# Kernel optimization log

Measured on AMD Instinct MI355X. Metric: run time of the kernel, lower is better.

The kernel has to match this reference:

```python
import jax, jax.numpy as jnp
import numpy as np

WS = 7      # window size
SS = 3      # shift size = WS // 2
NH = 12     # num heads
EPS = 1e-5  # LayerNorm eps


def _ln(x, g, b):
    m = jnp.mean(x, axis=-1, keepdims=True)
    v = jnp.var(x, axis=-1, keepdims=True)
    return (x - m) * jax.lax.rsqrt(v + EPS) * g + b


def _rel_index(ws):
    # relative position index (N, N), N = ws*ws (static, numpy)
    coords = np.stack(np.meshgrid(np.arange(ws), np.arange(ws), indexing='ij')).reshape(2, -1)
    rel = (coords[:, :, None] - coords[:, None, :]).transpose(1, 2, 0).copy()
    rel[:, :, 0] += ws - 1
    rel[:, :, 1] += ws - 1
    rel[:, :, 0] *= 2 * ws - 1
    return rel.sum(-1)


def _attn_mask(H, W, ws, ss):
    # SW-MSA mask (nW, N, N): -100 where tokens come from different shifted regions
    img = np.zeros((H, W), np.float32)
    cnt = 0
    sls = (slice(0, -ws), slice(-ws, -ss), slice(-ss, None))
    for hs in sls:
        for wsl in sls:
            img[hs, wsl] = cnt
            cnt += 1
    win = img.reshape(H // ws, ws, W // ws, ws).transpose(0, 2, 1, 3).reshape(-1, ws * ws)
    d = win[:, None, :] - win[:, :, None]
    return np.where(d != 0, -100.0, 0.0).astype(np.float32)


def _forward(x, rel_bias_table, qkv_w, qkv_b, proj_w, proj_b,
             norm1_w, norm1_b, norm2_w, norm2_b,
             mlp_w1, mlp_b1, mlp_w2, mlp_b2, h, w):
    B, L, C = x.shape
    ws, ss, nH = WS, SS, NH
    hd = C // nH
    N = ws * ws
    scale = hd ** -0.5
    nWh, nWw = h // ws, w // ws
    nW = nWh * nWw

    shortcut = x
    y = _ln(x, norm1_w, norm1_b).reshape(B, h, w, C)
    # cyclic shift (SW-MSA)
    y = jnp.roll(y, (-ss, -ss), axis=(1, 2))
    # window partition -> (B*nW, N, C)
    y = y.reshape(B, nWh, ws, nWw, ws, C).transpose(0, 1, 3, 2, 4, 5).reshape(-1, N, C)

    qkv = (y @ qkv_w + qkv_b).reshape(-1, N, 3, nH, hd).transpose(2, 0, 3, 1, 4)
    q, k, v = qkv[0] * scale, qkv[1], qkv[2]  # (Bw, nH, N, hd)

    attn = jnp.einsum('bhnd,bhmd->bhnm', q, k)  # (Bw, nH, N, N)
    # learned relative position bias
    idx = jnp.asarray(_rel_index(ws))  # (N, N)
    bias = rel_bias_table[idx].transpose(2, 0, 1)[None]  # (1, nH, N, N)
    attn = attn + bias
    # shifted-window mask
    mask = jnp.asarray(_attn_mask(h, w, ws, ss))  # (nW, N, N)
    attn = attn.reshape(B, nW, nH, N, N) + mask[None, :, None]
    attn = jax.nn.softmax(attn.reshape(-1, nH, N, N), axis=-1)

    out = jnp.einsum('bhnm,bhmd->bhnd', attn, v).transpose(0, 2, 1, 3).reshape(-1, N, C)
    out = out @ proj_w + proj_b
    # window reverse + un-shift
    out = out.reshape(B, nWh, nWw, ws, ws, C).transpose(0, 1, 3, 2, 4, 5).reshape(B, h, w, C)
    out = jnp.roll(out, (ss, ss), axis=(1, 2)).reshape(B, L, C)

    x = shortcut + out
    y2 = _ln(x, norm2_w, norm2_b)
    mlp = jax.nn.gelu(y2 @ mlp_w1 + mlp_b1, approximate=False) @ mlp_w2 + mlp_b2
    return x + mlp


def setup_inputs() -> dict:
    key = jax.random.key(0)
    ks = jax.random.split(key, 8)
    B, H, W, C = 32, 56, 56, 384
    hid = int(C * 4.0)
    ws, nH = WS, NH
    inp = {
        'x': jax.random.normal(ks[0], (B, H * W, C), jnp.float32),
        'rel_bias_table': 0.02 * jax.random.normal(ks[1], ((2 * ws - 1) * (2 * ws - 1), nH), jnp.float32),
        'qkv_w': 0.02 * jax.random.normal(ks[2], (C, 3 * C), jnp.float32),
        'qkv_b': jnp.zeros((3 * C,), jnp.float32),
        'proj_w': 0.02 * jax.random.normal(ks[3], (C, C), jnp.float32),
        'proj_b': jnp.zeros((C,), jnp.float32),
        'norm1_w': jnp.ones((C,), jnp.float32),
        'norm1_b': jnp.zeros((C,), jnp.float32),
        'norm2_w': jnp.ones((C,), jnp.float32),
        'norm2_b': jnp.zeros((C,), jnp.float32),
        'mlp_w1': 0.02 * jax.random.normal(ks[4], (C, hid), jnp.float32),
        'mlp_b1': jnp.zeros((hid,), jnp.float32),
        'mlp_w2': 0.02 * jax.random.normal(ks[5], (hid, C), jnp.float32),
        'mlp_b2': jnp.zeros((C,), jnp.float32),
        'h': H,
        'w': W,
    }
    return inp


def reference(x, rel_bias_table, qkv_w, qkv_b, proj_w, proj_b,
              norm1_w, norm1_b, norm2_w, norm2_b,
              mlp_w1, mlp_b1, mlp_w2, mlp_b2, h, w):
    return _forward(x, rel_bias_table, qkv_w, qkv_b, proj_w, proj_b,
                    norm1_w, norm1_b, norm2_w, norm2_b,
                    mlp_w1, mlp_b1, mlp_w2, mlp_b2, h, w)
```

## Files before the change

### kernel.cpp

```cpp
#include <hip/hip_runtime.h>

typedef unsigned short u16;
typedef unsigned int u32;
typedef short s8v __attribute__((ext_vector_type(8)));
typedef float f4 __attribute__((ext_vector_type(4)));

#define GL16(g, l) __builtin_amdgcn_global_load_lds((const __attribute__((address_space(1))) u32*)(g), (__attribute__((address_space(3))) u32*)(l), 16, 0, 0)

__device__ __forceinline__ u16 f2bf(float f){
  u32 u = __builtin_bit_cast(u32, f);
  u32 r = u + 0x7fffu + ((u >> 16) & 1u);
  return (u16)(r >> 16);
}

__device__ __forceinline__ u32 pk_bf16(float lo, float hi){
  u32 r;
  asm("v_cvt_pk_bf16_f32 %0, %1, %2" : "=v"(r) : "v"(lo), "v"(hi));
  return r;
}

__device__ __forceinline__ float gelu_f(float x){
  float y = fabsf(x) * 0.70710678118654752f;
  float t = __builtin_amdgcn_rcpf(1.f + 0.3275911f*y);
  float p = ((((1.061405429f*t - 1.453152027f)*t + 1.421413741f)*t - 0.284496736f)*t + 0.254829592f)*t;
  float er = 1.f - p*__expf(-y*y);
  er = copysignf(er, x);
  return 0.5f*x*(1.f + er);
}

__device__ __forceinline__ int win_to_src(int orow){
  int wi = orow / 49;
  int n  = orow - wi*49;
  int b  = wi >> 6;
  int wq = wi & 63;
  int wh = wq >> 3, ww = wq & 7;
  int r = n / 7, c = n - r*7;
  int hh = wh*7 + r + 3; if (hh >= 56) hh -= 56;
  int wp = ww*7 + c + 3; if (wp >= 56) wp -= 56;
  return (b*56 + hh)*56 + wp;
}

__global__ void sentinel_kernel(float* o){ o[0] = 1.0e9f; }

__global__ void transpose_cast(const float* __restrict__ in, u16* __restrict__ out,
                               int K, int N, float scale, int scale_lim){
  __shared__ float tile[16][17];
  int kb = blockIdx.x*16, nb = blockIdx.y*16;
  int tx = threadIdx.x, ty = threadIdx.y;
  int k = kb + ty, n = nb + tx;
  tile[ty][tx] = (k < K && n < N) ? in[(size_t)k*N + n] : 0.f;
  __syncthreads();
  int on = nb + ty, ok = kb + tx;
  if (on < N && ok < K){
    float v = tile[tx][ty];
    if (on < scale_lim) v *= scale;
    out[(size_t)on*K + ok] = f2bf(v);
  }
}

__global__ void scale_bias(const float* __restrict__ in, float* __restrict__ out,
                           int n, float s, int lim){
  int i = blockIdx.x*256 + threadIdx.x;
  if (i < n) out[i] = in[i] * (i < lim ? s : 1.f);
}

__global__ void build_biasmask(const float* __restrict__ table, float* __restrict__ bm){
  int wq = blockIdx.x, h = blockIdx.y;
  int wh = wq >> 3, ww = wq & 7;
  float* o = bm + (size_t)(wq*12 + h) * 4096;
  for (int i = threadIdx.x; i < 4096; i += 256){
    int m = i >> 6, n = i & 63;
    float v;
    if (m < 49 && n < 49){
      int rm = m/7, cm = m - rm*7;
      int rn = n/7, cn = n - rn*7;
      int idx = (rm - rn + 6)*13 + (cm - cn + 6);
      v = table[idx*12 + h];
      int ym = wh*7 + rm, xm = ww*7 + cm;
      int yn = wh*7 + rn, xn = ww*7 + cn;
      int lm = (ym < 49 ? 0 : (ym < 53 ? 1 : 2))*3 + (xm < 49 ? 0 : (xm < 53 ? 1 : 2));
      int ln = (yn < 49 ? 0 : (yn < 53 ? 1 : 2))*3 + (xn < 49 ? 0 : (xn < 53 ? 1 : 2));
      if (lm != ln) v += -100.f;
    } else {
      v = -1e9f;
    }
    o[i] = v;
  }
}

template<bool GATHER>
__global__ __launch_bounds__(256) void ln_kernel(const float* __restrict__ x,
    const float* __restrict__ g, const float* __restrict__ b,
    u16* __restrict__ y, int nrows)
{
  int row = blockIdx.x*4 + (threadIdx.x >> 6);
  int lane = threadIdx.x & 63;
  if (row >= nrows) return;
  int src = GATHER ? win_to_src(row) : row;
  const float* xr = x + (size_t)src*384;
  float v[6];
  float s = 0.f, s2 = 0.f;
  #pragma unroll
  for (int p = 0; p < 3; p++){
    float2 t = *(const float2*)(xr + p*128 + lane*2);
    v[p*2] = t.x; v[p*2+1] = t.y;
    s += t.x + t.y; s2 += t.x*t.x + t.y*t.y;
  }
  #pragma unroll
  for (int off = 32; off; off >>= 1){
    s  += __shfl_xor(s,  off);
    s2 += __shfl_xor(s2, off);
  }
  float mean = s * (1.f/384.f);
  float var  = s2 * (1.f/384.f) - mean*mean;
  float rs   = rsqrtf(var + 1e-5f);
  u16* yr = y + (size_t)row*384;
  #pragma unroll
  for (int p = 0; p < 3; p++){
    int c = p*128 + lane*2;
    float a0 = (v[p*2]   - mean)*rs*g[c]   + b[c];
    float a1 = (v[p*2+1] - mean)*rs*g[c+1] + b[c+1];
    *(u32*)(yr + c) = pk_bf16(a0, a1);
  }
}

template<int MODE, int NF>
__global__ __launch_bounds__(256) void gemm_bf16(
    const u16* __restrict__ A, const u16* __restrict__ Bt,
    const float* __restrict__ bias, const float* __restrict__ resid,
    void* __restrict__ outp, int K, int N, int gn)
{
  constexpr int TN = NF * 32;
  __shared__ u16 As[2][128*64];
  __shared__ u16 Bs[2][TN*64];
  const int tid  = threadIdx.x;
  const int lane = tid & 63, wv = tid >> 6;
  const int wr = wv >> 1, wc = wv & 1;
  const int l15 = lane & 15, lhi = lane >> 4;
  const int sw  = l15 & 7;

  int total = gridDim.x;
  int flat  = blockIdx.x;
  int swz   = flat;
  if ((total & 7) == 0){
    int cpx = total >> 3;
    swz = (flat & 7)*cpx + (flat >> 3);
  }
  int bm = swz / gn, bn = swz - bm*gn;
  const size_t m0 = (size_t)bm * 128;
  const int n0 = bn * TN;

  f4 acc[4][NF] = {};

  auto stage = [&](int buf, int kt){
    #pragma unroll
    for (int it = 0; it < 4; it++){
      int c = it*256 + tid;
      int row = c >> 3;
      int col = (((c & 7) ^ (row & 7))) * 8;
      const u16* ga = A + (m0 + (size_t)row)*K + kt*64 + col;
      GL16(ga, &As[buf][(it*256 + wv*64)*8]);
    }
    #pragma unroll
    for (int it = 0; it < NF; it++){
      int c = it*256 + tid;
      int row = c >> 3;
      int col = (((c & 7) ^ (row & 7))) * 8;
      const u16* gb = Bt + ((size_t)n0 + row)*K + kt*64 + col;
      GL16(gb, &Bs[buf][(it*256 + wv*64)*8]);
    }
  };

  const int nk = K >> 6;
  stage(0, 0);
  for (int kt = 0; kt < nk; kt++){
    const int cur = kt & 1;
    if (kt + 1 < nk){
      stage(cur ^ 1, kt + 1);
      asm volatile("s_waitcnt vmcnt(8)" ::: "memory");
    } else {
      asm volatile("s_waitcnt vmcnt(0)" ::: "memory");
    }
    __builtin_amdgcn_s_barrier();
    #pragma unroll
    for (int kk = 0; kk < 2; kk++){
      s8v a[4], bb[NF];
      #pragma unroll
      for (int mi = 0; mi < 4; mi++)
        a[mi] = *(const s8v*)&As[cur][(wr*64 + mi*16 + l15)*64 + ((kk*4 + lhi) ^ sw)*8];
      #pragma unroll
      for (int ni = 0; ni < NF; ni++)
        bb[ni] = *(const s8v*)&Bs[cur][(wc*NF*16 + ni*16 + l15)*64 + ((kk*4 + lhi) ^ sw)*8];
      #pragma unroll
      for (int mi = 0; mi < 4; mi++)
        #pragma unroll
        for (int ni = 0; ni < NF; ni++)
          acc[mi][ni] = __builtin_amdgcn_mfma_f32_16x16x32_bf16(bb[ni], a[mi], acc[mi][ni], 0, 0, 0);
    }
    asm volatile("s_waitcnt lgkmcnt(0)" ::: "memory");
    __builtin_amdgcn_s_barrier();
  }

  #pragma unroll
  for (int mi = 0; mi < 4; mi++){
    int m = (int)m0 + wr*64 + mi*16 + l15;
    int src = 0;
    if constexpr (MODE == 1) src = win_to_src(m);
    #pragma unroll
    for (int ni = 0; ni < NF; ni++){
      int n = n0 + wc*NF*16 + ni*16 + lhi*4;
      f4 v = acc[mi][ni];
      float4 b4 = *(const float4*)(bias + n);
      v[0] += b4.x; v[1] += b4.y; v[2] += b4.z; v[3] += b4.w;
      if constexpr (MODE == 0){
        uint2 pk; pk.x = pk_bf16(v[0], v[1]); pk.y = pk_bf16(v[2], v[3]);
        *(uint2*)((u16*)outp + (size_t)m*N + n) = pk;
      } else if constexpr (MODE == 1){
        const float4 r4 = *(const float4*)(resid + (size_t)src*384 + n);
        float4 o4; o4.x = v[0]+r4.x; o4.y = v[1]+r4.y; o4.z = v[2]+r4.z; o4.w = v[3]+r4.w;
        *(float4*)((float*)outp + (size_t)src*384 + n) = o4;
      } else if constexpr (MODE == 2){
        uint2 pk;
        pk.x = pk_bf16(gelu_f(v[0]), gelu_f(v[1]));
        pk.y = pk_bf16(gelu_f(v[2]), gelu_f(v[3]));
        *(uint2*)((u16*)outp + (size_t)m*N + n) = pk;
      } else {
        float4* o = (float4*)((float*)outp + (size_t)m*N + n);
        float4 c4 = *o;
        c4.x += v[0]; c4.y += v[1]; c4.z += v[2]; c4.w += v[3];
        *o = c4;
      }
    }
  }
}

__global__ __launch_bounds__(256) void attn_kernel(
    const u16* __restrict__ qkv, const float* __restrict__ bm, u16* __restrict__ ao)
{
  const int wi = blockIdx.x;
  const int hg = blockIdx.y;
  const int wv = threadIdx.x >> 6, lane = threadIdx.x & 63;
  const int h = hg*4 + wv;
  const int l15 = lane & 15, lhi = lane >> 4;
  const int wq = wi & 63;

  __shared__ u16 Plds[4][64*72];
  __shared__ u16 Vlds[4][32*72];

  const size_t base = (size_t)wi * 49 * 1152;

  for (int i = 0; i < 32; i++){
    int idx = i*64 + lane;
    int n = idx >> 5, d = idx & 31;
    u16 v = (n < 49) ? qkv[base + (size_t)n*1152 + 768 + h*32 + d] : (u16)0;
    Vlds[wv][d*72 + n] = v;
  }

  s8v aQ[4], bK[4];
  s8v z8 = (s8v)0;
  #pragma unroll
  for (int mi = 0; mi < 4; mi++){
    int rowq = mi*16 + l15;
    aQ[mi] = (rowq < 49) ? *(const s8v*)&qkv[base + (size_t)rowq*1152 +   0 + h*32 + lhi*8] : z8;
    bK[mi] = (rowq < 49) ? *(const s8v*)&qkv[base + (size_t)rowq*1152 + 384 + h*32 + lhi*8] : z8;
  }
  f4 zf = {0.f, 0.f, 0.f, 0.f};
  f4 s[4][4];
  #pragma unroll
  for (int mi = 0; mi < 4; mi++)
    #pragma unroll
    for (int ni = 0; ni < 4; ni++)
      s[mi][ni] = __builtin_amdgcn_mfma_f32_16x16x32_bf16(aQ[mi], bK[ni], zf, 0, 0, 0);

  const float* bmp = bm + (size_t)(wq*12 + h) * 4096;
  #pragma unroll
  for (int mi = 0; mi < 4; mi++)
    #pragma unroll
    for (int ni = 0; ni < 4; ni++)
      #pragma unroll
      for (int r = 0; r < 4; r++){
        int m = mi*16 + lhi*4 + r, n = ni*16 + l15;
        s[mi][ni][r] += bmp[m*64 + n];
      }

  #pragma unroll
  for (int mi = 0; mi < 4; mi++){
    #pragma unroll
    for (int r = 0; r < 4; r++){
      float mx = fmaxf(fmaxf(s[mi][0][r], s[mi][1][r]), fmaxf(s[mi][2][r], s[mi][3][r]));
      mx = fmaxf(mx, __shfl_xor(mx, 1));
      mx = fmaxf(mx, __shfl_xor(mx, 2));
      mx = fmaxf(mx, __shfl_xor(mx, 4));
      mx = fmaxf(mx, __shfl_xor(mx, 8));
      float sum = 0.f;
      #pragma unroll
      for (int ni = 0; ni < 4; ni++){
        float p = __expf(s[mi][ni][r] - mx);
        s[mi][ni][r] = p; sum += p;
      }
      sum += __shfl_xor(sum, 1);
      sum += __shfl_xor(sum, 2);
      sum += __shfl_xor(sum, 4);
      sum += __shfl_xor(sum, 8);
      float inv = 1.f / sum;
      #pragma unroll
      for (int ni = 0; ni < 4; ni++) s[mi][ni][r] *= inv;
    }
  }

  #pragma unroll
  for (int mi = 0; mi < 4; mi++)
    #pragma unroll
    for (int ni = 0; ni < 4; ni++)
      #pragma unroll
      for (int r = 0; r < 4; r++){
        int m = mi*16 + lhi*4 + r, n = ni*16 + l15;
        Plds[wv][m*72 + n] = f2bf(s[mi][ni][r]);
      }
  __syncthreads();

  f4 o[4][2] = {};
  #pragma unroll
  for (int ks = 0; ks < 2; ks++){
    s8v aP[4], bV[2];
    #pragma unroll
    for (int mi = 0; mi < 4; mi++)
      aP[mi] = *(const s8v*)&Plds[wv][(mi*16 + l15)*72 + ks*32 + lhi*8];
    #pragma unroll
    for (int di = 0; di < 2; di++)
      bV[di] = *(const s8v*)&Vlds[wv][(di*16 + l15)*72 + ks*32 + lhi*8];
    #pragma unroll
    for (int mi = 0; mi < 4; mi++)
      #pragma unroll
      for (int di = 0; di < 2; di++)
        o[mi][di] = __builtin_amdgcn_mfma_f32_16x16x32_bf16(aP[mi], bV[di], o[mi][di], 0, 0, 0);
  }

  #pragma unroll
  for (int mi = 0; mi < 4; mi++)
    #pragma unroll
    for (int di = 0; di < 2; di++)
      #pragma unroll
      for (int r = 0; r < 4; r++){
        int m = mi*16 + lhi*4 + r;
        if (m < 49){
          int d = di*16 + l15;
          ao[((size_t)wi*49 + m)*384 + h*32 + d] = f2bf(o[mi][di][r]);
        }
      }
}

extern "C" void kernel_launch(void* const* d_in, const int* in_sizes, int n_in,
                              void* d_out, int out_size, void* d_ws, size_t ws_size,
                              hipStream_t stream)
{
  const float* x      = (const float*)d_in[0];
  const float* table  = (const float*)d_in[1];
  const float* qkv_w  = (const float*)d_in[2];
  const float* qkv_b  = (const float*)d_in[3];
  const float* proj_w = (const float*)d_in[4];
  const float* proj_b = (const float*)d_in[5];
  const float* n1w    = (const float*)d_in[6];
  const float* n1b    = (const float*)d_in[7];
  const float* n2w    = (const float*)d_in[8];
  const float* n2b    = (const float*)d_in[9];
  const float* w1     = (const float*)d_in[10];
  const float* b1     = (const float*)d_in[11];
  const float* w2     = (const float*)d_in[12];
  const float* b2     = (const float*)d_in[13];
  float* out = (float*)d_out;

  const size_t M = 100352;
  const float SC = 0.17677669529663689f;

  const size_t R1 = M * 1536 * 2;
  const size_t R2 = M * 384 * 2;
  const size_t R3 = (size_t)64*12*64*64*4;
  const size_t WT = (size_t)(1152*384 + 384*384 + 1536*384 + 384*1536) * 2;
  const size_t BB = 1152 * 4;
  const size_t needed = R1 + R2 + R3 + WT + BB;
  if (ws_size < needed){
    sentinel_kernel<<<1, 1, 0, stream>>>(out);
    return;
  }

  char* p = (char*)d_ws;
  u16*   qkvbuf = (u16*)p;
  u16*   ybuf   = (u16*)(p + R1);
  float* bmbuf  = (float*)(p + R1 + R2);
  u16*   qkvT   = (u16*)(p + R1 + R2 + R3);
  u16*   projT  = qkvT  + (size_t)1152*384;
  u16*   w1T    = projT + (size_t)384*384;
  u16*   w2T    = w1T   + (size_t)1536*384;
  float* qkvb_s = (float*)(p + R1 + R2 + R3 + WT);

  transpose_cast<<<dim3(24, 72),  dim3(16,16), 0, stream>>>(qkv_w,  qkvT, 384, 1152, SC, 384);
  transpose_cast<<<dim3(24, 24),  dim3(16,16), 0, stream>>>(proj_w, projT, 384, 384, 1.f, 0);
  transpose_cast<<<dim3(24, 96),  dim3(16,16), 0, stream>>>(w1,     w1T,  384, 1536, 1.f, 0);
  transpose_cast<<<dim3(96, 24),  dim3(16,16), 0, stream>>>(w2,     w2T,  1536, 384, 1.f, 0);
  scale_bias<<<5, 256, 0, stream>>>(qkv_b, qkvb_s, 1152, SC, 384);
  build_biasmask<<<dim3(64, 12), 256, 0, stream>>>(table, bmbuf);

  ln_kernel<true><<<M/4, 256, 0, stream>>>(x, n1w, n1b, ybuf, (int)M);

  gemm_bf16<0,4><<<784*9, 256, 0, stream>>>(ybuf, qkvT, qkvb_s, nullptr, qkvbuf, 384, 1152, 9);

  attn_kernel<<<dim3(2048, 3), 256, 0, stream>>>(qkvbuf, bmbuf, ybuf);

  gemm_bf16<1,4><<<784*3, 256, 0, stream>>>(ybuf, projT, proj_b, x, out, 384, 384, 3);

  ln_kernel<false><<<M/4, 256, 0, stream>>>(out, n2w, n2b, ybuf, (int)M);

  gemm_bf16<2,4><<<784*12, 256, 0, stream>>>(ybuf, w1T, b1, nullptr, qkvbuf, 384, 1536, 12);

  gemm_bf16<3,4><<<784*3, 256, 0, stream>>>(qkvbuf, w2T, b2, nullptr, out, 1536, 384, 3);
}
```

Baseline: 994.7 us.

## Replace 128-row GEMM tiles with 256x256 tiles using 512-thread blocks

Rewrites the bf16 MFMA GEMM to compute 256x256 output tiles per 512-thread block, with each of 8 waves owning a 128x64 sub-tile, in place of the old 128xTN tiles on 256 threads. Transposed weight buffers are padded to multiples of 256 rows, and epilogue stores skip columns at or beyond the real output width. The goal is higher operand reuse per LDS load and fewer blocks. In exchange, the projection and MLP-down GEMMs spend about a quarter of their MFMA work on padding columns, and QKV spends about a tenth. The 128 KB of LDS per block likely also limits occupancy to one block per CU.

Measured after the change: 1.160 ms. +16.6%, slower.

```diff
diff --git a/kernel.cpp b/kernel.cpp
--- a/kernel.cpp
+++ b/kernel.cpp
@@ -124,18 +124,17 @@
   }
 }
 
-template<int MODE, int NF>
-__global__ __launch_bounds__(256) void gemm_bf16(
+template<int MODE>
+__global__ __launch_bounds__(512, 2) void gemm256(
     const u16* __restrict__ A, const u16* __restrict__ Bt,
     const float* __restrict__ bias, const float* __restrict__ resid,
-    void* __restrict__ outp, int K, int N, int gn)
+    void* __restrict__ outp, int K, int Nout, int gn)
 {
-  constexpr int TN = NF * 32;
-  __shared__ u16 As[2][128*64];
-  __shared__ u16 Bs[2][TN*64];
+  __shared__ u16 As[2][256*64];
+  __shared__ u16 Bs[2][256*64];
   const int tid  = threadIdx.x;
   const int lane = tid & 63, wv = tid >> 6;
-  const int wr = wv >> 1, wc = wv & 1;
+  const int wm = wv >> 2, wn = wv & 3;
   const int l15 = lane & 15, lhi = lane >> 4;
   const int sw  = l15 & 7;
 
@@ -147,27 +146,27 @@
     swz = (flat & 7)*cpx + (flat >> 3);
   }
   int bm = swz / gn, bn = swz - bm*gn;
-  const size_t m0 = (size_t)bm * 128;
-  const int n0 = bn * TN;
-
-  f4 acc[4][NF] = {};
+  const size_t m0 = (size_t)bm * 256;
+  const int n0 = bn * 256;
+
+  f4 acc[8][4] = {};
 
   auto stage = [&](int buf, int kt){
     #pragma unroll
     for (int it = 0; it < 4; it++){
-      int c = it*256 + tid;
+      int c = it*512 + tid;
       int row = c >> 3;
-      int col = (((c & 7) ^ (row & 7))) * 8;
+      int col = ((c & 7) ^ (row & 7)) * 8;
       const u16* ga = A + (m0 + (size_t)row)*K + kt*64 + col;
-      GL16(ga, &As[buf][(it*256 + wv*64)*8]);
-    }
-    #pragma unroll
-    for (int it = 0; it < NF; it++){
-      int c = it*256 + tid;
+      GL16(ga, &As[buf][(it*512 + wv*64)*8]);
+    }
+    #pragma unroll
+    for (int it = 0; it < 4; it++){
+      int c = it*512 + tid;
       int row = c >> 3;
-      int col = (((c & 7) ^ (row & 7))) * 8;
+      int col = ((c & 7) ^ (row & 7)) * 8;
       const u16* gb = Bt + ((size_t)n0 + row)*K + kt*64 + col;
-      GL16(gb, &Bs[buf][(it*256 + wv*64)*8]);
+      GL16(gb, &Bs[buf][(it*512 + wv*64)*8]);
     }
   };
 
@@ -184,17 +183,17 @@
     __builtin_amdgcn_s_barrier();
     #pragma unroll
     for (int kk = 0; kk < 2; kk++){
-      s8v a[4], bb[NF];
-      #pragma unroll
-      for (int mi = 0; mi < 4; mi++)
-        a[mi] = *(const s8v*)&As[cur][(wr*64 + mi*16 + l15)*64 + ((kk*4 + lhi) ^ sw)*8];
-      #pragma unroll
-      for (int ni = 0; ni < NF; ni++)
-        bb[ni] = *(const s8v*)&Bs[cur][(wc*NF*16 + ni*16 + l15)*64 + ((kk*4 + lhi) ^ sw)*8];
-      #pragma unroll
-      for (int mi = 0; mi < 4; mi++)
+      s8v a[8], bb[4];
+      #pragma unroll
+      for (int mi = 0; mi < 8; mi++)
+        a[mi] = *(const s8v*)&As[cur][(wm*128 + mi*16 + l15)*64 + ((kk*4 + lhi) ^ sw)*8];
+      #pragma unroll
+      for (int ni = 0; ni < 4; ni++)
+        bb[ni] = *(const s8v*)&Bs[cur][(wn*64 + ni*16 + l15)*64 + ((kk*4 + lhi) ^ sw)*8];
+      #pragma unroll
+      for (int mi = 0; mi < 8; mi++)
         #pragma unroll
-        for (int ni = 0; ni < NF; ni++)
+        for (int ni = 0; ni < 4; ni++)
           acc[mi][ni] = __builtin_amdgcn_mfma_f32_16x16x32_bf16(bb[ni], a[mi], acc[mi][ni], 0, 0, 0);
     }
     asm volatile("s_waitcnt lgkmcnt(0)" ::: "memory");
@@ -202,19 +201,20 @@
   }
 
   #pragma unroll
-  for (int mi = 0; mi < 4; mi++){
-    int m = (int)m0 + wr*64 + mi*16 + l15;
+  for (int mi = 0; mi < 8; mi++){
+    int m = (int)m0 + wm*128 + mi*16 + l15;
     int src = 0;
     if constexpr (MODE == 1) src = win_to_src(m);
     #pragma unroll
-    for (int ni = 0; ni < NF; ni++){
-      int n = n0 + wc*NF*16 + ni*16 + lhi*4;
+    for (int ni = 0; ni < 4; ni++){
+      int n = n0 + wn*64 + ni*16 + lhi*4;
+      if (n >= Nout) continue;
       f4 v = acc[mi][ni];
       float4 b4 = *(const float4*)(bias + n);
       v[0] += b4.x; v[1] += b4.y; v[2] += b4.z; v[3] += b4.w;
       if constexpr (MODE == 0){
         uint2 pk; pk.x = pk_bf16(v[0], v[1]); pk.y = pk_bf16(v[2], v[3]);
-        *(uint2*)((u16*)outp + (size_t)m*N + n) = pk;
+        *(uint2*)((u16*)outp + (size_t)m*Nout + n) = pk;
       } else if constexpr (MODE == 1){
         const float4 r4 = *(const float4*)(resid + (size_t)src*384 + n);
         float4 o4; o4.x = v[0]+r4.x; o4.y = v[1]+r4.y; o4.z = v[2]+r4.z; o4.w = v[3]+r4.w;
@@ -223,9 +223,9 @@
         uint2 pk;
         pk.x = pk_bf16(gelu_f(v[0]), gelu_f(v[1]));
         pk.y = pk_bf16(gelu_f(v[2]), gelu_f(v[3]));
-        *(uint2*)((u16*)outp + (size_t)m*N + n) = pk;
+        *(uint2*)((u16*)outp + (size_t)m*Nout + n) = pk;
       } else {
-        float4* o = (float4*)((float*)outp + (size_t)m*N + n);
+        float4* o = (float4*)((float*)outp + (size_t)m*Nout + n);
         float4 c4 = *o;
         c4.x += v[0]; c4.y += v[1]; c4.z += v[2]; c4.w += v[3];
         *o = c4;
@@ -376,7 +376,7 @@
   const size_t R1 = M * 1536 * 2;
   const size_t R2 = M * 384 * 2;
   const size_t R3 = (size_t)64*12*64*64*4;
-  const size_t WT = (size_t)(1152*384 + 384*384 + 1536*384 + 384*1536) * 2;
+  const size_t WT = (size_t)(1280*384 + 512*384 + 1536*384 + 512*1536) * 2;
   const size_t BB = 1152 * 4;
   const size_t needed = R1 + R2 + R3 + WT + BB;
   if (ws_size < needed){
@@ -389,8 +389,8 @@
   u16*   ybuf   = (u16*)(p + R1);
   float* bmbuf  = (float*)(p + R1 + R2);
   u16*   qkvT   = (u16*)(p + R1 + R2 + R3);
-  u16*   projT  = qkvT  + (size_t)1152*384;
-  u16*   w1T    = projT + (size_t)384*384;
+  u16*   projT  = qkvT  + (size_t)1280*384;
+  u16*   w1T    = projT + (size_t)512*384;
   u16*   w2T    = w1T   + (size_t)1536*384;
   float* qkvb_s = (float*)(p + R1 + R2 + R3 + WT);
 
@@ -403,15 +403,15 @@
 
   ln_kernel<true><<<M/4, 256, 0, stream>>>(x, n1w, n1b, ybuf, (int)M);
 
-  gemm_bf16<0,4><<<784*9, 256, 0, stream>>>(ybuf, qkvT, qkvb_s, nullptr, qkvbuf, 384, 1152, 9);
+  gemm256<0><<<392*5, 512, 0, stream>>>(ybuf, qkvT, qkvb_s, nullptr, qkvbuf, 384, 1152, 5);
 
   attn_kernel<<<dim3(2048, 3), 256, 0, stream>>>(qkvbuf, bmbuf, ybuf);
 
-  gemm_bf16<1,4><<<784*3, 256, 0, stream>>>(ybuf, projT, proj_b, x, out, 384, 384, 3);
+  gemm256<1><<<392*2, 512, 0, stream>>>(ybuf, projT, proj_b, x, out, 384, 384, 2);
 
   ln_kernel<false><<<M/4, 256, 0, stream>>>(out, n2w, n2b, ybuf, (int)M);
 
-  gemm_bf16<2,4><<<784*12, 256, 0, stream>>>(ybuf, w1T, b1, nullptr, qkvbuf, 384, 1536, 12);
-
-  gemm_bf16<3,4><<<784*3, 256, 0, stream>>>(qkvbuf, w2T, b2, nullptr, out, 1536, 384, 3);
-}
+  gemm256<2><<<392*6, 512, 0, stream>>>(ybuf, w1T, b1, nullptr, qkvbuf, 384, 1536, 6);
+
+  gemm256<3><<<392*2, 512, 0, stream>>>(qkvbuf, w2T, b2, nullptr, out, 1536, 384, 2);
+}
```

## Add A-stationary GEMM keeping 64-row A tile in LDS across all N tiles

Applied to the files above, without the earlier changes.

Adds a new GEMM kernel for K=384 that loads a full 64x384 A block into LDS once, then sweeps every 128-column output tile while double-buffering B tiles. It replaces the QKV, proj and fc1 GEMMs, aiming to cut repeated A reads from global memory and to use larger 512-thread blocks. The workspace for weight layouts grows. Each block now runs a long serial loop over the N tiles with smaller per-wave tiles (32x32), which may lower MFMA efficiency and the number of blocks in flight per CU.

Result: slower. 1.022 ms (+2.7%).

```diff
diff --git a/kernel.cpp b/kernel.cpp
--- a/kernel.cpp
+++ b/kernel.cpp
@@ -122,6 +122,126 @@
     float a1 = (v[p*2+1] - mean)*rs*g[c+1] + b[c+1];
     *(u32*)(yr + c) = pk_bf16(a0, a1);
   }
+}
+
+template<int MODE, int GN>
+__global__ __launch_bounds__(512, 4) void gemmA(
+    const u16* __restrict__ A, const u16* __restrict__ Bt,
+    const float* __restrict__ bias, const float* __restrict__ resid,
+    void* __restrict__ outp)
+{
+  constexpr int K = 384, NK = 6;
+  constexpr int Nout = GN * 128;
+  __shared__ u16 Al[64*384];
+  __shared__ u16 Bl[2][128*64];
+  const int tid  = threadIdx.x;
+  const int lane = tid & 63, wv = tid >> 6;
+  const int wm = wv >> 2, wn = wv & 3;
+  const int l15 = lane & 15, lhi = lane >> 4;
+  const int sw  = l15 & 7;
+
+  int total = gridDim.x;
+  int flat  = blockIdx.x;
+  int swz   = flat;
+  if ((total & 7) == 0){
+    int cpx = total >> 3;
+    swz = (flat & 7)*cpx + (flat >> 3);
+  }
+  const size_t m0 = (size_t)swz * 64;
+
+  #pragma unroll
+  for (int it = 0; it < 6; it++){
+    int idx = it*512 + tid;
+    int row = idx / 48;
+    int c   = idx - row*48;
+    const u16* g = A + (m0 + (size_t)row)*K + ((c ^ (row & 7)) * 8);
+    GL16(g, &Al[(it*512 + wv*64)*8]);
+  }
+  const u16* pB0;
+  const u16* pB1;
+  {
+    int idx0 = tid,        r0 = idx0 >> 3, c0 = idx0 & 7;
+    int idx1 = 512 + tid,  r1 = idx1 >> 3, c1 = idx1 & 7;
+    pB0 = Bt + (size_t)r0*K + ((c0 ^ (r0 & 7))*8);
+    pB1 = Bt + (size_t)r1*K + ((c1 ^ (r1 & 7))*8);
+  }
+  GL16(pB0, &Bl[0][(wv*64)*8]);
+  GL16(pB1, &Bl[0][(512 + wv*64)*8]);
+  asm volatile("s_waitcnt vmcnt(0)" ::: "memory");
+  __builtin_amdgcn_s_barrier();
+
+  const int arow = wm*32;
+  int src0 = 0, src1 = 0;
+  if constexpr (MODE == 1){
+    src0 = win_to_src((int)m0 + arow + l15);
+    src1 = win_to_src((int)m0 + arow + 16 + l15);
+  }
+
+  size_t pOff = 0;
+  for (int p = 0; p < GN; p++){
+    f4 acc[2][2] = {};
+    const size_t pOffNext = (p + 1 < GN) ? pOff + (size_t)128*K : 0;
+    #pragma unroll
+    for (int kt = 0; kt < NK; kt++){
+      const int cur = kt & 1;
+      size_t off = (kt + 1 < NK) ? (pOff + (size_t)(kt+1)*64) : pOffNext;
+      GL16(pB0 + off, &Bl[cur^1][(wv*64)*8]);
+      GL16(pB1 + off, &Bl[cur^1][(512 + wv*64)*8]);
+      asm volatile("s_waitcnt vmcnt(2)" ::: "memory");
+      __builtin_amdgcn_s_barrier();
+
+      s8v a[2][2], b[2][2];
+      #pragma unroll
+      for (int mi = 0; mi < 2; mi++)
+        #pragma unroll
+        for (int kk = 0; kk < 2; kk++)
+          a[mi][kk] = *(const s8v*)&Al[(arow + mi*16 + l15)*384 + (((kt*8 + kk*4 + lhi) ^ sw))*8];
+      #pragma unroll
+      for (int ni = 0; ni < 2; ni++)
+        #pragma unroll
+        for (int kk = 0; kk < 2; kk++)
+          b[ni][kk] = *(const s8v*)&Bl[cur][(wn*32 + ni*16 + l15)*64 + (((kk*4 + lhi) ^ sw))*8];
+      #pragma unroll
+      for (int kk = 0; kk < 2; kk++)
+        #pragma unroll
+        for (int mi = 0; mi < 2; mi++)
+          #pragma unroll
+          for (int ni = 0; ni < 2; ni++)
+            acc[mi][ni] = __builtin_amdgcn_mfma_f32_16x16x32_bf16(
+                b[ni][kk], a[mi][kk], acc[mi][ni], 0, 0, 0);
+
+      asm volatile("s_waitcnt lgkmcnt(0)" ::: "memory");
+      __builtin_amdgcn_s_barrier();
+    }
+
+    #pragma unroll
+    for (int mi = 0; mi < 2; mi++){
+      int m = (int)m0 + arow + mi*16 + l15;
+      int src = (mi == 0) ? src0 : src1;
+      #pragma unroll
+      for (int ni = 0; ni < 2; ni++){
+        int n = p*128 + wn*32 + ni*16 + lhi*4;
+        f4 v = acc[mi][ni];
+        float4 b4 = *(const float4*)(bias + n);
+        v[0] += b4.x; v[1] += b4.y; v[2] += b4.z; v[3] += b4.w;
+        if constexpr (MODE == 0){
+          uint2 pk; pk.x = pk_bf16(v[0], v[1]); pk.y = pk_bf16(v[2], v[3]);
+          *(uint2*)((u16*)outp + (size_t)m*Nout + n) = pk;
+        } else if constexpr (MODE == 1){
+          const float4 r4 = *(const float4*)(resid + (size_t)src*384 + n);
+          float4 o4; o4.x = v[0]+r4.x; o4.y = v[1]+r4.y; o4.z = v[2]+r4.z; o4.w = v[3]+r4.w;
+          *(float4*)((float*)outp + (size_t)src*384 + n) = o4;
+        } else {
+          uint2 pk;
+          pk.x = pk_bf16(gelu_f(v[0]), gelu_f(v[1]));
+          pk.y = pk_bf16(gelu_f(v[2]), gelu_f(v[3]));
+          *(uint2*)((u16*)outp + (size_t)m*Nout + n) = pk;
+        }
+      }
+    }
+    pOff = pOffNext;
+  }
+  asm volatile("s_waitcnt vmcnt(0)" ::: "memory");
 }
 
 template<int MODE, int NF>
@@ -376,7 +496,7 @@
   const size_t R1 = M * 1536 * 2;
   const size_t R2 = M * 384 * 2;
   const size_t R3 = (size_t)64*12*64*64*4;
-  const size_t WT = (size_t)(1152*384 + 384*384 + 1536*384 + 384*1536) * 2;
+  const size_t WT = (size_t)(1280*384 + 512*384 + 1536*384 + 512*1536) * 2;
   const size_t BB = 1152 * 4;
   const size_t needed = R1 + R2 + R3 + WT + BB;
   if (ws_size < needed){
@@ -389,8 +509,8 @@
   u16*   ybuf   = (u16*)(p + R1);
   float* bmbuf  = (float*)(p + R1 + R2);
   u16*   qkvT   = (u16*)(p + R1 + R2 + R3);
-  u16*   projT  = qkvT  + (size_t)1152*384;
-  u16*   w1T    = projT + (size_t)384*384;
+  u16*   projT  = qkvT  + (size_t)1280*384;
+  u16*   w1T    = projT + (size_t)512*384;
   u16*   w2T    = w1T   + (size_t)1536*384;
   float* qkvb_s = (float*)(p + R1 + R2 + R3 + WT);
 
@@ -403,15 +523,15 @@
 
   ln_kernel<true><<<M/4, 256, 0, stream>>>(x, n1w, n1b, ybuf, (int)M);
 
-  gemm_bf16<0,4><<<784*9, 256, 0, stream>>>(ybuf, qkvT, qkvb_s, nullptr, qkvbuf, 384, 1152, 9);
+  gemmA<0, 9><<<1568, 512, 0, stream>>>(ybuf, qkvT, qkvb_s, nullptr, qkvbuf);
 
   attn_kernel<<<dim3(2048, 3), 256, 0, stream>>>(qkvbuf, bmbuf, ybuf);
 
-  gemm_bf16<1,4><<<784*3, 256, 0, stream>>>(ybuf, projT, proj_b, x, out, 384, 384, 3);
+  gemmA<1, 3><<<1568, 512, 0, stream>>>(ybuf, projT, proj_b, x, out);
 
   ln_kernel<false><<<M/4, 256, 0, stream>>>(out, n2w, n2b, ybuf, (int)M);
 
-  gemm_bf16<2,4><<<784*12, 256, 0, stream>>>(ybuf, w1T, b1, nullptr, qkvbuf, 384, 1536, 12);
+  gemmA<2, 12><<<1568, 512, 0, stream>>>(ybuf, w1T, b1, nullptr, qkvbuf);
 
   gemm_bf16<3,4><<<784*3, 256, 0, stream>>>(qkvbuf, w2T, b2, nullptr, out, 1536, 384, 3);
 }
```

## Halve GEMM K-tile, store bias-mask as bf16, vectorize V staging in attention

Applied to the files above, without the earlier changes.

Cuts the GEMM K tile from 64 to 32. This halves the LDS footprint so more blocks can be resident per CU, but doubles the number of barriers per K loop. The combined relative-position-bias and shift-mask table is now stored in bf16, halving its memory traffic in the attention kernel at some precision cost. V is loaded with 16-byte vector reads before being transposed into LDS, replacing scalar 2-byte loads.

After: 1.054 ms. 6.0% more time.

```diff
diff --git a/kernel.cpp b/kernel.cpp
--- a/kernel.cpp
+++ b/kernel.cpp
@@ -11,6 +11,10 @@
   u32 u = __builtin_bit_cast(u32, f);
   u32 r = u + 0x7fffu + ((u >> 16) & 1u);
   return (u16)(r >> 16);
+}
+__device__ __forceinline__ float bf2f(u16 u){
+  u32 x = ((u32)u) << 16;
+  return __builtin_bit_cast(float, x);
 }
 
 __device__ __forceinline__ u32 pk_bf16(float lo, float hi){
@@ -64,10 +68,10 @@
   if (i < n) out[i] = in[i] * (i < lim ? s : 1.f);
 }
 
-__global__ void build_biasmask(const float* __restrict__ table, float* __restrict__ bm){
+__global__ void build_biasmask(const float* __restrict__ table, u16* __restrict__ bm){
   int wq = blockIdx.x, h = blockIdx.y;
   int wh = wq >> 3, ww = wq & 7;
-  float* o = bm + (size_t)(wq*12 + h) * 4096;
+  u16* o = bm + (size_t)(wq*12 + h) * 4096;
   for (int i = threadIdx.x; i < 4096; i += 256){
     int m = i >> 6, n = i & 63;
     float v;
@@ -84,7 +88,7 @@
     } else {
       v = -1e9f;
     }
-    o[i] = v;
+    o[i] = f2bf(v);
   }
 }
 
@@ -131,13 +135,13 @@
     void* __restrict__ outp, int K, int N, int gn)
 {
   constexpr int TN = NF * 32;
-  __shared__ u16 As[2][128*64];
-  __shared__ u16 Bs[2][TN*64];
+  __shared__ u16 As[2][128*32];
+  __shared__ u16 Bs[2][TN*32];
   const int tid  = threadIdx.x;
   const int lane = tid & 63, wv = tid >> 6;
   const int wr = wv >> 1, wc = wv & 1;
   const int l15 = lane & 15, lhi = lane >> 4;
-  const int sw  = l15 & 7;
+  const int sw2 = l15 & 3;
 
   int total = gridDim.x;
   int flat  = blockIdx.x;
@@ -154,49 +158,46 @@
 
   auto stage = [&](int buf, int kt){
     #pragma unroll
-    for (int it = 0; it < 4; it++){
+    for (int it = 0; it < 2; it++){
       int c = it*256 + tid;
-      int row = c >> 3;
-      int col = (((c & 7) ^ (row & 7))) * 8;
-      const u16* ga = A + (m0 + (size_t)row)*K + kt*64 + col;
+      int row = c >> 2;
+      int col = ((c & 3) ^ (row & 3)) * 8;
+      const u16* ga = A + (m0 + (size_t)row)*K + kt*32 + col;
       GL16(ga, &As[buf][(it*256 + wv*64)*8]);
     }
     #pragma unroll
-    for (int it = 0; it < NF; it++){
+    for (int it = 0; it < 2; it++){
       int c = it*256 + tid;
-      int row = c >> 3;
-      int col = (((c & 7) ^ (row & 7))) * 8;
-      const u16* gb = Bt + ((size_t)n0 + row)*K + kt*64 + col;
+      int row = c >> 2;
+      int col = ((c & 3) ^ (row & 3)) * 8;
+      const u16* gb = Bt + ((size_t)n0 + row)*K + kt*32 + col;
       GL16(gb, &Bs[buf][(it*256 + wv*64)*8]);
     }
   };
 
-  const int nk = K >> 6;
+  const int nk = K >> 5;
   stage(0, 0);
   for (int kt = 0; kt < nk; kt++){
     const int cur = kt & 1;
     if (kt + 1 < nk){
       stage(cur ^ 1, kt + 1);
-      asm volatile("s_waitcnt vmcnt(8)" ::: "memory");
+      asm volatile("s_waitcnt vmcnt(4)" ::: "memory");
     } else {
       asm volatile("s_waitcnt vmcnt(0)" ::: "memory");
     }
     __builtin_amdgcn_s_barrier();
-    #pragma unroll
-    for (int kk = 0; kk < 2; kk++){
-      s8v a[4], bb[NF];
-      #pragma unroll
-      for (int mi = 0; mi < 4; mi++)
-        a[mi] = *(const s8v*)&As[cur][(wr*64 + mi*16 + l15)*64 + ((kk*4 + lhi) ^ sw)*8];
+    s8v a[4], bb[NF];
+    #pragma unroll
+    for (int mi = 0; mi < 4; mi++)
+      a[mi] = *(const s8v*)&As[cur][(wr*64 + mi*16 + l15)*32 + (lhi ^ sw2)*8];
+    #pragma unroll
+    for (int ni = 0; ni < NF; ni++)
+      bb[ni] = *(const s8v*)&Bs[cur][(wc*NF*16 + ni*16 + l15)*32 + (lhi ^ sw2)*8];
+    #pragma unroll
+    for (int mi = 0; mi < 4; mi++)
       #pragma unroll
       for (int ni = 0; ni < NF; ni++)
-        bb[ni] = *(const s8v*)&Bs[cur][(wc*NF*16 + ni*16 + l15)*64 + ((kk*4 + lhi) ^ sw)*8];
-      #pragma unroll
-      for (int mi = 0; mi < 4; mi++)
-        #pragma unroll
-        for (int ni = 0; ni < NF; ni++)
-          acc[mi][ni] = __builtin_amdgcn_mfma_f32_16x16x32_bf16(bb[ni], a[mi], acc[mi][ni], 0, 0, 0);
-    }
+        acc[mi][ni] = __builtin_amdgcn_mfma_f32_16x16x32_bf16(bb[ni], a[mi], acc[mi][ni], 0, 0, 0);
     asm volatile("s_waitcnt lgkmcnt(0)" ::: "memory");
     __builtin_amdgcn_s_barrier();
   }
@@ -235,7 +236,7 @@
 }
 
 __global__ __launch_bounds__(256) void attn_kernel(
-    const u16* __restrict__ qkv, const float* __restrict__ bm, u16* __restrict__ ao)
+    const u16* __restrict__ qkv, const u16* __restrict__ bm, u16* __restrict__ ao)
 {
   const int wi = blockIdx.x;
   const int hg = blockIdx.y;
@@ -248,16 +249,19 @@
   __shared__ u16 Vlds[4][32*72];
 
   const size_t base = (size_t)wi * 49 * 1152;
-
-  for (int i = 0; i < 32; i++){
-    int idx = i*64 + lane;
-    int n = idx >> 5, d = idx & 31;
-    u16 v = (n < 49) ? qkv[base + (size_t)n*1152 + 768 + h*32 + d] : (u16)0;
-    Vlds[wv][d*72 + n] = v;
+  s8v z8 = (s8v)0;
+
+  #pragma unroll
+  for (int i = 0; i < 4; i++){
+    int n  = i*16 + (lane >> 2);
+    int d8 = (lane & 3)*8;
+    s8v v = (n < 49) ? *(const s8v*)&qkv[base + (size_t)n*1152 + 768 + h*32 + d8] : z8;
+    #pragma unroll
+    for (int j = 0; j < 8; j++)
+      Vlds[wv][(d8 + j)*72 + n] = (u16)v[j];
   }
 
   s8v aQ[4], bK[4];
-  s8v z8 = (s8v)0;
   #pragma unroll
   for (int mi = 0; mi < 4; mi++){
     int rowq = mi*16 + l15;
@@ -272,7 +276,7 @@
     for (int ni = 0; ni < 4; ni++)
       s[mi][ni] = __builtin_amdgcn_mfma_f32_16x16x32_bf16(aQ[mi], bK[ni], zf, 0, 0, 0);
 
-  const float* bmp = bm + (size_t)(wq*12 + h) * 4096;
+  const u16* bmp = bm + (size_t)(wq*12 + h) * 4096;
   #pragma unroll
   for (int mi = 0; mi < 4; mi++)
     #pragma unroll
@@ -280,7 +284,7 @@
       #pragma unroll
       for (int r = 0; r < 4; r++){
         int m = mi*16 + lhi*4 + r, n = ni*16 + l15;
-        s[mi][ni][r] += bmp[m*64 + n];
+        s[mi][ni][r] += bf2f(bmp[m*64 + n]);
       }
 
   #pragma unroll
@@ -375,7 +379,7 @@
 
   const size_t R1 = M * 1536 * 2;
   const size_t R2 = M * 384 * 2;
-  const size_t R3 = (size_t)64*12*64*64*4;
+  const size_t R3 = (size_t)64*12*64*64*2;
   const size_t WT = (size_t)(1152*384 + 384*384 + 1536*384 + 384*1536) * 2;
   const size_t BB = 1152 * 4;
   const size_t needed = R1 + R2 + R3 + WT + BB;
@@ -387,7 +391,7 @@
   char* p = (char*)d_ws;
   u16*   qkvbuf = (u16*)p;
   u16*   ybuf   = (u16*)(p + R1);
-  float* bmbuf  = (float*)(p + R1 + R2);
+  u16*   bmbuf  = (u16*)(p + R1 + R2);
   u16*   qkvT   = (u16*)(p + R1 + R2 + R3);
   u16*   projT  = qkvT  + (size_t)1152*384;
   u16*   w1T    = projT + (size_t)384*384;
```
